# Performance work log

Hardware: AMD Instinct MI355X
Metric: run time of the kernel (lower is better)

The kernel has to match this reference:

```python
import jax, jax.numpy as jnp
import numpy as np

B, T, HOR = 4096, 128, 24
EH, DH, A = 64, 64, 32


def setup_inputs() -> dict:
    key = jax.random.key(0)
    ks = jax.random.split(key, 21)
    g = lambda k, shape, s=0.1: (jax.random.normal(k, shape, jnp.float32) * s)
    return {
        "x": jax.random.normal(ks[0], (B, T, 1), jnp.float32),
        # encoder GRUCell (input_size=1)
        "W_ih_e": g(ks[1], (3 * EH, 1)), "W_hh_e": g(ks[2], (3 * EH, EH)),
        "b_ih_e": g(ks[3], (3 * EH,)), "b_hh_e": g(ks[4], (3 * EH,)),
        # encoder input attention
        "W_e": g(ks[5], (A, EH)), "U_e": g(ks[6], (1, A)),
        "b_e": jnp.zeros((1, A), jnp.float32), "v_e": g(ks[7], (A,)),
        # decoder init
        "W_init": g(ks[8], (DH, EH)), "b_init": g(ks[9], (DH,)),
        # decoder GRUCell (input_size=1)
        "W_ih_d": g(ks[10], (3 * DH, 1)), "W_hh_d": g(ks[11], (3 * DH, DH)),
        "b_ih_d": g(ks[12], (3 * DH,)), "b_hh_d": g(ks[13], (3 * DH,)),
        # temporal attention
        "W_d": g(ks[14], (A, DH)), "U_d": g(ks[15], (A, EH)), "v_d": g(ks[16], (A,)),
        # output head
        "W_out": g(ks[17], (1, DH + EH)), "b_out": g(ks[18], (1,)),
        "y0": jnp.zeros((1,), jnp.float32),
    }


def _gru_cell(x, h, W_ih, W_hh, b_ih, b_hh):
    # PyTorch GRUCell semantics
    gi = x @ W_ih.T + b_ih  # (B, 3H)
    gh = h @ W_hh.T + b_hh
    ir, iz, inn = jnp.split(gi, 3, axis=1)
    hr, hz, hn = jnp.split(gh, 3, axis=1)
    r = jax.nn.sigmoid(ir + hr)
    z = jax.nn.sigmoid(iz + hz)
    n = jnp.tanh(inn + r * hn)
    return (1.0 - z) * n + z * h


def reference(x, W_ih_e, W_hh_e, b_ih_e, b_hh_e, W_e, U_e, b_e, v_e,
              W_init, b_init, W_ih_d, W_hh_d, b_ih_d, b_hh_d,
              W_d, U_d, v_d, W_out, b_out, y0):
    bsz = x.shape[0]

    def enc_step(h, x_t):  # x_t: (B, 1)
        h_proj = h @ W_e.T  # (B, A)
        attn = jnp.tanh(h_proj[:, None, :] + x_t[:, :, None] * U_e[None] + b_e[None])  # (B,1,A)
        scores = jnp.sum(attn * v_e, axis=2)  # (B, 1)
        alpha = jax.nn.softmax(scores, axis=1)
        h_new = _gru_cell(alpha * x_t, h, W_ih_e, W_hh_e, b_ih_e, b_hh_e)
        return h_new, h_new

    h0 = jnp.zeros((bsz, EH), x.dtype)
    h_T, Hs = jax.lax.scan(enc_step, h0, jnp.swapaxes(x, 0, 1))  # Hs: (T,B,EH)
    H = jnp.swapaxes(Hs, 0, 1)  # (B, T, EH)

    d0 = h_T @ W_init.T + b_init  # (B, DH)
    H_proj = jnp.einsum('bte,ae->bta', H, U_d)  # hoisted: constant across decoder steps
    dec_in0 = jnp.broadcast_to(y0[None, :], (bsz, 1))

    def dec_step(carry, _):
        d, dec_in = carry
        d = _gru_cell(dec_in, d, W_ih_d, W_hh_d, b_ih_d, b_hh_d)
        d_proj = d @ W_d.T  # (B, A)
        attn = jnp.tanh(d_proj[:, None, :] + H_proj)  # (B, T, A)
        beta = jax.nn.softmax(jnp.sum(attn * v_d, axis=2), axis=1)  # (B, T)
        ctx = jnp.einsum('bt,bte->be', beta, H)  # (B, EH)
        out = jnp.concatenate([d, ctx], axis=1) @ W_out.T + b_out  # (B, 1)
        return (d, out), out[:, 0]

    (_, _), outs = jax.lax.scan(dec_step, (d0, dec_in0), None, length=HOR)
    return outs.T  # (B, horizon)
```

## Files before the change

kernel.cpp:

```cpp
#include <hip/hip_runtime.h>
#include <math.h>

#define BATCH 4096
#define T 128
#define HOR 24

#define LOG2E 1.44269504088896f
#define C2    2.88539008177793f

typedef _Float16 half2_t __attribute__((ext_vector_type(2)));
typedef _Float16 half8   __attribute__((ext_vector_type(8)));
typedef float f2  __attribute__((ext_vector_type(2)));
typedef float f4v __attribute__((ext_vector_type(4)));

__device__ __forceinline__ float fexp2(float x){ return __builtin_amdgcn_exp2f(x); }
__device__ __forceinline__ float frcp(float x){ return __builtin_amdgcn_rcpf(x); }
__device__ __forceinline__ float fsig(float x){ return frcp(1.0f + fexp2(-LOG2E*x)); }
__device__ __forceinline__ float ftanh(float x){ return fmaf(-2.0f, frcp(1.0f + fexp2(C2*x)), 1.0f); }
__device__ __forceinline__ half2_t bch(unsigned u){ return __builtin_bit_cast(half2_t,u); }
__device__ __forceinline__ unsigned pk2(float a,float b){ return __builtin_bit_cast(unsigned, __builtin_amdgcn_cvt_pkrtz(a,b)); }
__device__ __forceinline__ unsigned pk2rne(float a,float b){
  half2_t h; h.x = (_Float16)a; h.y = (_Float16)b;
  return __builtin_bit_cast(unsigned, h);
}
__device__ __forceinline__ float fdot2f(half2_t a, half2_t b, float c){
#if __has_builtin(__builtin_amdgcn_fdot2)
  return __builtin_amdgcn_fdot2(a,b,c,false);
#else
  return fmaf((float)a.x,(float)b.x, fmaf((float)a.y,(float)b.y,c));
#endif
}
__device__ __forceinline__ f2 pkfma(f2 a, f2 b, f2 c){ return __builtin_elementwise_fma(a,b,c); }

template <int CTRL, int RMASK>
__device__ __forceinline__ float dpp_add(float v) {
  int s = __builtin_amdgcn_update_dpp(0, __builtin_bit_cast(int, v), CTRL, RMASK, 0xf, true);
  return v + __builtin_bit_cast(float, s);
}
__device__ __forceinline__ float wavesum_dpp(float v) {
  v = dpp_add<0x111, 0xf>(v);
  v = dpp_add<0x112, 0xf>(v);
  v = dpp_add<0x114, 0xf>(v);
  v = dpp_add<0x118, 0xf>(v);
  v = dpp_add<0x142, 0xa>(v);
  v = dpp_add<0x143, 0xc>(v);
  return v;
}
__device__ __forceinline__ float rdl63(float v){
  return __builtin_bit_cast(float, __builtin_amdgcn_readlane(__builtin_bit_cast(int, v), 63));
}

#define WG_BARRIER_LDS() do {                                   \
    asm volatile("s_waitcnt lgkmcnt(0)" ::: "memory");          \
    __builtin_amdgcn_s_barrier();                               \
  } while (0)

__device__ __forceinline__ void gru_mv(const _Float16* hrow,
    const unsigned* wr_r, const unsigned* wr_z, const unsigned* wr_n,
    float& ar0, float& ar1, float& az0, float& az1, float& an0, float& an1)
{
  const uint4* hq = (const uint4*)hrow;
  #pragma unroll
  for (int q = 0; q < 8; ++q) {
    uint4 hv = hq[q];
    ar0 = fdot2f(bch(hv.x), bch(wr_r[4*q+0]), ar0);
    az0 = fdot2f(bch(hv.x), bch(wr_z[4*q+0]), az0);
    an0 = fdot2f(bch(hv.x), bch(wr_n[4*q+0]), an0);
    ar1 = fdot2f(bch(hv.y), bch(wr_r[4*q+1]), ar1);
    az1 = fdot2f(bch(hv.y), bch(wr_z[4*q+1]), az1);
    an1 = fdot2f(bch(hv.y), bch(wr_n[4*q+1]), an1);
    ar0 = fdot2f(bch(hv.z), bch(wr_r[4*q+2]), ar0);
    az0 = fdot2f(bch(hv.z), bch(wr_z[4*q+2]), az0);
    an0 = fdot2f(bch(hv.z), bch(wr_n[4*q+2]), an0);
    ar1 = fdot2f(bch(hv.w), bch(wr_r[4*q+3]), ar1);
    az1 = fdot2f(bch(hv.w), bch(wr_z[4*q+3]), az1);
    an1 = fdot2f(bch(hv.w), bch(wr_n[4*q+3]), an1);
  }
}

__device__ __forceinline__ float proj_dot(const _Float16* base, const unsigned* udr)
{
  float acc = 0.f;
  const uint4* hb = (const uint4*)base;
  #pragma unroll
  for (int q = 0; q < 4; ++q) {
    uint4 hv = hb[q];
    acc = fdot2f(bch(hv.x), bch(udr[4*q+0]), acc);
    acc = fdot2f(bch(hv.y), bch(udr[4*q+1]), acc);
    acc = fdot2f(bch(hv.z), bch(udr[4*q+2]), acc);
    acc = fdot2f(bch(hv.w), bch(udr[4*q+3]), acc);
  }
  return acc;
}

__device__ __forceinline__ half8 cvt8(f4v a, f4v b){
  half8 h;
  h[0]=(_Float16)a.x; h[1]=(_Float16)a.y; h[2]=(_Float16)a.z; h[3]=(_Float16)a.w;
  h[4]=(_Float16)b.x; h[5]=(_Float16)b.y; h[6]=(_Float16)b.z; h[7]=(_Float16)b.w;
  return h;
}

__global__ __launch_bounds__(256, 1)
void darnn_enc(const float* __restrict__ x,
               const float* __restrict__ W_ih_e, const float* __restrict__ W_hh_e,
               const float* __restrict__ b_ih_e, const float* __restrict__ b_hh_e,
               const float* __restrict__ U_d, const float* __restrict__ W_out,
               unsigned* __restrict__ hpG, float* __restrict__ hTG)
{
  const int tid = threadIdx.x;
  const int w = tid >> 6;
  const int l = tid & 63;
  const int c = l & 15;
  const int q = l >> 4;
  const int e0 = blockIdx.x * 16;
  const int m0 = 16*w + 4*q;

  __shared__ __align__(16) _Float16 He[2][16*72];
  __shared__ __align__(16) unsigned xw[16*65];
  __shared__ __align__(16) unsigned ehC[2][16*273];

  for (int idx = tid; idx < 16*64; idx += 256) {
    int e = idx >> 6, j = idx & 63;
    f2 g = ((const f2*)(x + (size_t)(e0+e)*T))[j];
    xw[e*65 + j] = pk2(g.x, g.y);
  }
  for (int idx = tid; idx < 576; idx += 256) ((unsigned*)He[0])[idx] = 0;

  half8 Ar[2], Az[2], An[2];
  #pragma unroll
  for (int kap = 0; kap < 2; ++kap) {
    const f4v* pr = (const f4v*)(W_hh_e + (size_t)(16*w + c)*64       + 32*kap + 8*q);
    const f4v* pz = (const f4v*)(W_hh_e + (size_t)(64 + 16*w + c)*64  + 32*kap + 8*q);
    const f4v* pn = (const f4v*)(W_hh_e + (size_t)(128 + 16*w + c)*64 + 32*kap + 8*q);
    Ar[kap] = cvt8(pr[0], pr[1]);
    Az[kap] = cvt8(pz[0], pz[1]);
    An[kap] = cvt8(pn[0], pn[1]);
  }
  half8 AX[2] = {{0,0,0,0,0,0,0,0},{0,0,0,0,0,0,0,0}};
  if (w < 2) {
    #pragma unroll
    for (int kap = 0; kap < 2; ++kap) {
      const f4v* p = (const f4v*)(U_d + (size_t)(16*w + c)*64 + 32*kap + 8*q);
      AX[kap] = cvt8(p[0] * C2, p[1] * C2);
    }
  } else if (w == 2 && c == 0) {
    #pragma unroll
    for (int kap = 0; kap < 2; ++kap) {
      const f4v* p = (const f4v*)(W_out + 64 + 32*kap + 8*q);
      AX[kap] = cvt8(p[0], p[1]);
    }
  }
  f4v wih0 = *(const f4v*)(W_ih_e + m0);
  f4v wih1 = *(const f4v*)(W_ih_e + 64 + m0);
  f4v wih2 = *(const f4v*)(W_ih_e + 128 + m0);
  f4v bb0  = *(const f4v*)(b_ih_e + m0)      + *(const f4v*)(b_hh_e + m0);
  f4v bb1  = *(const f4v*)(b_ih_e + 64 + m0) + *(const f4v*)(b_hh_e + 64 + m0);
  f4v bi2  = *(const f4v*)(b_ih_e + 128 + m0);
  f4v bh2  = *(const f4v*)(b_hh_e + 128 + m0);
  f4v hreg = {0,0,0,0};
  const f4v z4 = {0,0,0,0};

  __syncthreads();

  #pragma unroll 1
  for (int t = 0; t < T; ++t) {
    if ((t & 15) == 1 && t > 16) {
      int cidx = (t - 17) >> 4;
      const unsigned* sbuf = ehC[cidx & 1];
      int t0 = cidx << 4;
      #pragma unroll
      for (int it = 0; it < 17; ++it) {
        int idx = tid + it*256;
        int e = idx / 272;
        int o = idx - e*272;
        hpG[(size_t)(e0+e)*2176 + t0*17 + o] = sbuf[e*273 + o];
      }
    }
    const _Float16* Hc = He[t & 1];
    half8 B0 = __builtin_bit_cast(half8, *(const uint4*)(Hc + c*72 + 8*q));
    half8 B1 = __builtin_bit_cast(half8, *(const uint4*)(Hc + c*72 + 32 + 8*q));
    if (t > 0) {
      unsigned* eb = ehC[((t-1) >> 4) & 1] + c*273 + ((t-1) & 15)*17;
      if (w < 2) {
        f4v cu = __builtin_amdgcn_mfma_f32_16x16x32_f16(AX[0], B0, z4, 0,0,0);
        cu     = __builtin_amdgcn_mfma_f32_16x16x32_f16(AX[1], B1, cu, 0,0,0);
        float x0 = fexp2(fminf(cu[0], 15.5f));
        float x1 = fexp2(fminf(cu[1], 15.5f));
        float x2 = fexp2(fminf(cu[2], 15.5f));
        float x3 = fexp2(fminf(cu[3], 15.5f));
        eb[8*w + 2*q]   = pk2rne(x0, x1);
        eb[8*w + 2*q+1] = pk2rne(x2, x3);
      } else if (w == 2) {
        f4v cw = __builtin_amdgcn_mfma_f32_16x16x32_f16(AX[0], B0, z4, 0,0,0);
        cw     = __builtin_amdgcn_mfma_f32_16x16x32_f16(AX[1], B1, cw, 0,0,0);
        if (q == 0) ((float*)eb)[16] = cw[0];
      }
    }
    f4v gr = __builtin_amdgcn_mfma_f32_16x16x32_f16(Ar[0], B0, z4, 0,0,0);
    gr     = __builtin_amdgcn_mfma_f32_16x16x32_f16(Ar[1], B1, gr, 0,0,0);
    f4v gz = __builtin_amdgcn_mfma_f32_16x16x32_f16(Az[0], B0, z4, 0,0,0);
    gz     = __builtin_amdgcn_mfma_f32_16x16x32_f16(Az[1], B1, gz, 0,0,0);
    f4v gn = __builtin_amdgcn_mfma_f32_16x16x32_f16(An[0], B0, z4, 0,0,0);
    gn     = __builtin_amdgcn_mfma_f32_16x16x32_f16(An[1], B1, gn, 0,0,0);
    float xc = (float)((const _Float16*)xw)[c*130 + t];
    f4v hn;
    #pragma unroll
    for (int i = 0; i < 4; ++i) {
      float r  = fsig(fmaf(xc, wih0[i], bb0[i]) + gr[i]);
      float zf = fsig(fmaf(xc, wih1[i], bb1[i]) + gz[i]);
      float n  = ftanh(fmaf(xc, wih2[i], bi2[i]) + r*(gn[i] + bh2[i]));
      float h  = fmaf(zf, hreg[i] - n, n);
      hreg[i] = h;
      hn[i] = h;
    }
    uint2 wv; wv.x = pk2(hn[0], hn[1]); wv.y = pk2(hn[2], hn[3]);
    *(uint2*)(He[(t+1)&1] + c*72 + m0) = wv;
    WG_BARRIER_LDS();
  }
  {
    const _Float16* Hc = He[0];
    half8 B0 = __builtin_bit_cast(half8, *(const uint4*)(Hc + c*72 + 8*q));
    half8 B1 = __builtin_bit_cast(half8, *(const uint4*)(Hc + c*72 + 32 + 8*q));
    unsigned* eb = ehC[1] + c*273 + 15*17;
    if (w < 2) {
      f4v cu = __builtin_amdgcn_mfma_f32_16x16x32_f16(AX[0], B0, z4, 0,0,0);
      cu     = __builtin_amdgcn_mfma_f32_16x16x32_f16(AX[1], B1, cu, 0,0,0);
      float x0 = fexp2(fminf(cu[0], 15.5f));
      float x1 = fexp2(fminf(cu[1], 15.5f));
      float x2 = fexp2(fminf(cu[2], 15.5f));
      float x3 = fexp2(fminf(cu[3], 15.5f));
      eb[8*w + 2*q]   = pk2rne(x0, x1);
      eb[8*w + 2*q+1] = pk2rne(x2, x3);
    } else if (w == 2) {
      f4v cw = __builtin_amdgcn_mfma_f32_16x16x32_f16(AX[0], B0, z4, 0,0,0);
      cw     = __builtin_amdgcn_mfma_f32_16x16x32_f16(AX[1], B1, cw, 0,0,0);
      if (q == 0) ((float*)eb)[16] = cw[0];
    }
  }
  WG_BARRIER_LDS();
  {
    const unsigned* sbuf = ehC[1];
    #pragma unroll
    for (int it = 0; it < 17; ++it) {
      int idx = tid + it*256;
      int e = idx / 272;
      int o = idx - e*272;
      hpG[(size_t)(e0+e)*2176 + 112*17 + o] = sbuf[e*273 + o];
    }
  }
  #pragma unroll
  for (int i = 0; i < 4; ++i)
    hTG[(size_t)(e0 + c)*64 + m0 + i] = hreg[i];
}

__global__ __launch_bounds__(128, 2)
void darnn_dec(const float* __restrict__ W_init, const float* __restrict__ b_init,
               const float* __restrict__ W_ih_d, const float* __restrict__ W_hh_d,
               const float* __restrict__ b_ih_d, const float* __restrict__ b_hh_d,
               const float* __restrict__ W_d, const float* __restrict__ v_d,
               const float* __restrict__ W_out, const float* __restrict__ b_out,
               const float* __restrict__ y0,
               const unsigned* __restrict__ hpG, const float* __restrict__ hTG,
               float* __restrict__ out)
{
  const int tid = threadIdx.x;
  const int wid = tid >> 6;
  const int l   = tid & 63;
  const int bA  = 4*blockIdx.x + 2*wid;
  const int bB  = bA + 1;
  const int a    = l & 31;
  const int half = l >> 5;

  __shared__ __align__(16) unsigned char smem[36928];
  unsigned char* wbp = smem + wid*18464;
  unsigned* hpA   = (unsigned*)wbp;
  unsigned* hpB   = (unsigned*)(wbp + 8704);
  _Float16* ringA = (_Float16*)(wbp + 17408);
  _Float16* ringB = (_Float16*)(wbp + 17536);
  float*    dpA   = (float*)(wbp + 17664);
  float*    dpB   = (float*)(wbp + 17792);
  float*    hTA   = (float*)(wbp + 17920);
  float*    hTB   = (float*)(wbp + 18176);

  {
    const uint4* sA = (const uint4*)(hpG + (size_t)bA * 2176);
    const uint4* sB = (const uint4*)(hpG + (size_t)bB * 2176);
    #pragma unroll
    for (int it = 0; it < 8; ++it) {
      ((uint4*)hpA)[it*64 + l] = sA[it*64 + l];
      ((uint4*)hpB)[it*64 + l] = sB[it*64 + l];
    }
    const unsigned* rA = hpG + (size_t)bA*2176 + 2048;
    const unsigned* rB = hpG + (size_t)bB*2176 + 2048;
    hpA[2048 + l] = rA[l];      hpA[2112 + l] = rA[64 + l];
    hpB[2048 + l] = rB[l];      hpB[2112 + l] = rB[64 + l];
  }
  hTA[l] = hTG[(size_t)bA*64 + l];
  hTB[l] = hTG[(size_t)bB*64 + l];

  unsigned wr_r[32], wr_z[32], wr_n[32];
  {
    const f4v* wp = (const f4v*)W_hh_d;
    #pragma unroll
    for (int k = 0; k < 16; ++k) {
      f4v vr = wp[l*16 + k];
      f4v vz = wp[(64 + l)*16 + k];
      f4v vn = wp[(128 + l)*16 + k];
      wr_r[2*k] = pk2(vr.x, vr.y); wr_r[2*k+1] = pk2(vr.z, vr.w);
      wr_z[2*k] = pk2(vz.x, vz.y); wr_z[2*k+1] = pk2(vz.z, vz.w);
      wr_n[2*k] = pk2(vn.x, vn.y); wr_n[2*k+1] = pk2(vn.z, vn.w);
    }
  }
  float wih0 = W_ih_d[l], wih1 = W_ih_d[64+l], wih2 = W_ih_d[128+l];
  float bb0  = b_ih_d[l] + b_hh_d[l];
  float bb1  = b_ih_d[64+l] + b_hh_d[64+l];
  float bih2 = b_ih_d[128+l], bhh2 = b_hh_d[128+l];
  unsigned udr[16];
  {
    const f2* up = (const f2*)(W_d + a*64 + half*32);
    #pragma unroll
    for (int k = 0; k < 16; ++k) { f2 f = up[k]; udr[k] = pk2(f.x, f.y); }
  }
  float dprevA, dprevB;
  {
    const f4v* wi = (const f4v*)(W_init + l*64);
    const f4v* ga = (const f4v*)hTA;
    const f4v* gb = (const f4v*)hTB;
    f2 aa0={0,0}, aa1={0,0}, ba0={0,0}, ba1={0,0};
    #pragma unroll
    for (int k = 0; k < 16; ++k) {
      f4v wv = wi[k];
      f4v va = ga[k], vb = gb[k];
      aa0 = pkfma(wv.xy, va.xy, aa0);
      aa1 = pkfma(wv.zw, va.zw, aa1);
      ba0 = pkfma(wv.xy, vb.xy, ba0);
      ba1 = pkfma(wv.zw, vb.zw, ba1);
    }
    float bi = b_init[l];
    dprevA = bi + (aa0.x + aa0.y) + (aa1.x + aa1.y);
    dprevB = bi + (ba0.x + ba0.y) + (ba1.x + ba1.y);
  }
  float wout1 = W_out[l];
  float hw0A = __builtin_bit_cast(float, hpA[l*17 + 16]);
  float hw1A = __builtin_bit_cast(float, hpA[(64 + l)*17 + 16]);
  float hw0B = __builtin_bit_cast(float, hpB[l*17 + 16]);
  float hw1B = __builtin_bit_cast(float, hpB[(64 + l)*17 + 16]);
  float oprevA = y0[0], oprevB = y0[0];
  float bo = b_out[0];
  float c1;
  {
    float sv = v_d[a];
    sv += __shfl_xor(sv, 16); sv += __shfl_xor(sv, 8);
    sv += __shfl_xor(sv, 4);  sv += __shfl_xor(sv, 2); sv += __shfl_xor(sv, 1);
    c1 = LOG2E * sv;
  }
  ringA[l] = (_Float16)dprevA;
  ringB[l] = (_Float16)dprevB;

  const unsigned* hprA0 = hpA + l*17;
  const unsigned* hprA1 = hpA + (64 + l)*17;
  const unsigned* hprB0 = hpB + l*17;
  const unsigned* hprB1 = hpB + (64 + l)*17;

  #pragma unroll 1
  for (int s = 0; s < HOR; ++s) {
    float ar0A=0,ar1A=0,az0A=0,az1A=0,an0A=0,an1A=0;
    float ar0B=0,ar1B=0,az0B=0,az1B=0,an0B=0,an1B=0;
    gru_mv(ringA, wr_r, wr_z, wr_n, ar0A,ar1A,az0A,az1A,an0A,an1A);
    gru_mv(ringB, wr_r, wr_z, wr_n, ar0B,ar1B,az0B,az1B,an0B,an1B);
    float rA = fsig(fmaf(oprevA, wih0, bb0) + ar0A + ar1A);
    float zA = fsig(fmaf(oprevA, wih1, bb1) + az0A + az1A);
    float nA = ftanh(fmaf(oprevA, wih2, bih2) + rA * (an0A + an1A + bhh2));
    float dnewA = fmaf(zA, dprevA - nA, nA);
    float rB = fsig(fmaf(oprevB, wih0, bb0) + ar0B + ar1B);
    float zB = fsig(fmaf(oprevB, wih1, bb1) + az0B + az1B);
    float nB = ftanh(fmaf(oprevB, wih2, bih2) + rB * (an0B + an1B + bhh2));
    float dnewB = fmaf(zB, dprevB - nB, nB);
    dprevA = dnewA; dprevB = dnewB;
    ringA[l] = (_Float16)dnewA;
    ringB[l] = (_Float16)dnewB;
    {
      float accA = proj_dot(ringA + half*32, udr);
      float accB = proj_dot(ringB + half*32, udr);
      accA += __shfl_xor(accA, 32);
      accB += __shfl_xor(accB, 32);
      if (l < 32) {
        dpA[l] = fexp2(C2 * accA);
        dpB[l] = fexp2(C2 * accB);
      }
    }
    float rs0A = 0.f, rs1A = 0.f, rs0B = 0.f, rs1B = 0.f;
    #pragma unroll
    for (int j2 = 0; j2 < 8; ++j2) {
      f4v edA = *(const f4v*)&dpA[4*j2];
      f4v edB = *(const f4v*)&dpB[4*j2];
      half2_t haA0 = bch(hprA0[2*j2]), hbA0 = bch(hprA0[2*j2+1]);
      half2_t haA1 = bch(hprA1[2*j2]), hbA1 = bch(hprA1[2*j2+1]);
      half2_t haB0 = bch(hprB0[2*j2]), hbB0 = bch(hprB0[2*j2+1]);
      half2_t haB1 = bch(hprB1[2*j2]), hbB1 = bch(hprB1[2*j2+1]);
      float v0 = v_d[4*j2], v1 = v_d[4*j2+1], v2 = v_d[4*j2+2], v3 = v_d[4*j2+3];
      rs0A = fmaf(v0, frcp(fmaf(edA.x, (float)haA0.x, 1.0f)), rs0A);
      rs0B = fmaf(v0, frcp(fmaf(edB.x, (float)haB0.x, 1.0f)), rs0B);
      rs0A = fmaf(v1, frcp(fmaf(edA.y, (float)haA0.y, 1.0f)), rs0A);
      rs0B = fmaf(v1, frcp(fmaf(edB.y, (float)haB0.y, 1.0f)), rs0B);
      rs0A = fmaf(v2, frcp(fmaf(edA.z, (float)hbA0.x, 1.0f)), rs0A);
      rs0B = fmaf(v2, frcp(fmaf(edB.z, (float)hbB0.x, 1.0f)), rs0B);
      rs0A = fmaf(v3, frcp(fmaf(edA.w, (float)hbA0.y, 1.0f)), rs0A);
      rs0B = fmaf(v3, frcp(fmaf(edB.w, (float)hbB0.y, 1.0f)), rs0B);
      rs1A = fmaf(v0, frcp(fmaf(edA.x, (float)haA1.x, 1.0f)), rs1A);
      rs1B = fmaf(v0, frcp(fmaf(edB.x, (float)haB1.x, 1.0f)), rs1B);
      rs1A = fmaf(v1, frcp(fmaf(edA.y, (float)haA1.y, 1.0f)), rs1A);
      rs1B = fmaf(v1, frcp(fmaf(edB.y, (float)haB1.y, 1.0f)), rs1B);
      rs1A = fmaf(v2, frcp(fmaf(edA.z, (float)hbA1.x, 1.0f)), rs1A);
      rs1B = fmaf(v2, frcp(fmaf(edB.z, (float)hbB1.x, 1.0f)), rs1B);
      rs1A = fmaf(v3, frcp(fmaf(edA.w, (float)hbA1.y, 1.0f)), rs1A);
      rs1B = fmaf(v3, frcp(fmaf(edB.w, (float)hbB1.y, 1.0f)), rs1B);
    }
    float e0A = fexp2(fmaf(-C2, rs0A, c1));
    float e1A = fexp2(fmaf(-C2, rs1A, c1));
    float e0B = fexp2(fmaf(-C2, rs0B, c1));
    float e1B = fexp2(fmaf(-C2, rs1B, c1));
    float P0A = rdl63(wavesum_dpp(e0A + e1A));
    float P1A = rdl63(wavesum_dpp(fmaf(e0A, hw0A, e1A * hw1A)));
    float P2A = rdl63(wavesum_dpp(wout1 * dnewA));
    float P0B = rdl63(wavesum_dpp(e0B + e1B));
    float P1B = rdl63(wavesum_dpp(fmaf(e0B, hw0B, e1B * hw1B)));
    float P2B = rdl63(wavesum_dpp(wout1 * dnewB));
    float oA = fmaf(P1A, frcp(P0A), P2A + bo);
    float oB = fmaf(P1B, frcp(P0B), P2B + bo);
    if (l == 0) {
      out[(size_t)bA * HOR + s] = oA;
      out[(size_t)bB * HOR + s] = oB;
    }
    oprevA = oA; oprevB = oB;
  }
}

extern "C" void kernel_launch(void* const* d_in, const int* in_sizes, int n_in,
                              void* d_out, int out_size, void* d_ws, size_t ws_size,
                              hipStream_t stream) {
  const float* x      = (const float*)d_in[0];
  const float* W_ih_e = (const float*)d_in[1];
  const float* W_hh_e = (const float*)d_in[2];
  const float* b_ih_e = (const float*)d_in[3];
  const float* b_hh_e = (const float*)d_in[4];
  const float* W_init = (const float*)d_in[9];
  const float* b_init = (const float*)d_in[10];
  const float* W_ih_d = (const float*)d_in[11];
  const float* W_hh_d = (const float*)d_in[12];
  const float* b_ih_d = (const float*)d_in[13];
  const float* b_hh_d = (const float*)d_in[14];
  const float* W_d    = (const float*)d_in[15];
  const float* U_d    = (const float*)d_in[16];
  const float* v_d    = (const float*)d_in[17];
  const float* W_out  = (const float*)d_in[18];
  const float* b_out  = (const float*)d_in[19];
  const float* y0     = (const float*)d_in[20];
  float* outp = (float*)d_out;

  unsigned* hpG = (unsigned*)d_ws;
  float*    hTG = (float*)((char*)d_ws + (size_t)BATCH * 2176 * 4);

  darnn_enc<<<BATCH/16, 256, 0, stream>>>(x, W_ih_e, W_hh_e, b_ih_e, b_hh_e,
      U_d, W_out, hpG, hTG);
  darnn_dec<<<BATCH/4, 128, 0, stream>>>(W_init, b_init, W_ih_d, W_hh_d,
      b_ih_d, b_hh_d, W_d, v_d, W_out, b_out, y0, hpG, hTG, outp);
}
```

Baseline: 272.1 us.

## Collapse encoder workgroup to one wave computing all hidden tiles without barriers

The encoder now runs one 64-lane wave per 16-sequence block instead of four waves. That single wave does all four gate row tiles plus the attention-projection MFMAs, so the per-step workgroup barrier and the double-buffered hidden state disappear. The projected keys are written straight to global memory each step instead of being staged in LDS and flushed in 16-step chunks. In exchange, each wave's serial dependency chain per step grows about fourfold, CU occupancy drops to one wave, and the global stores become small and strided rather than coalesced.

```diff
diff --git a/kernel.cpp b/kernel.cpp
--- a/kernel.cpp
+++ b/kernel.cpp
@@ -23,6 +23,7 @@
   half2_t h; h.x = (_Float16)a; h.y = (_Float16)b;
   return __builtin_bit_cast(unsigned, h);
 }
+__device__ __forceinline__ float e2c(float v){ return fexp2(fminf(v, 15.5f)); }
 __device__ __forceinline__ float fdot2f(half2_t a, half2_t b, float c){
 #if __has_builtin(__builtin_amdgcn_fdot2)
   return __builtin_amdgcn_fdot2(a,b,c,false);
@@ -49,11 +50,6 @@
 __device__ __forceinline__ float rdl63(float v){
   return __builtin_bit_cast(float, __builtin_amdgcn_readlane(__builtin_bit_cast(int, v), 63));
 }
-
-#define WG_BARRIER_LDS() do {                                   \
-    asm volatile("s_waitcnt lgkmcnt(0)" ::: "memory");          \
-    __builtin_amdgcn_s_barrier();                               \
-  } while (0)
 
 __device__ __forceinline__ void gru_mv(const _Float16* hrow,
     const unsigned* wr_r, const unsigned* wr_z, const unsigned* wr_n,
@@ -100,157 +96,139 @@
   return h;
 }
 
-__global__ __launch_bounds__(256, 1)
+__global__ __launch_bounds__(64, 1)
 void darnn_enc(const float* __restrict__ x,
                const float* __restrict__ W_ih_e, const float* __restrict__ W_hh_e,
                const float* __restrict__ b_ih_e, const float* __restrict__ b_hh_e,
                const float* __restrict__ U_d, const float* __restrict__ W_out,
                unsigned* __restrict__ hpG, float* __restrict__ hTG)
 {
-  const int tid = threadIdx.x;
-  const int w = tid >> 6;
-  const int l = tid & 63;
+  const int l = threadIdx.x;
   const int c = l & 15;
   const int q = l >> 4;
   const int e0 = blockIdx.x * 16;
-  const int m0 = 16*w + 4*q;
-
-  __shared__ __align__(16) _Float16 He[2][16*72];
+
+  __shared__ __align__(16) unsigned He[16*68];
   __shared__ __align__(16) unsigned xw[16*65];
-  __shared__ __align__(16) unsigned ehC[2][16*273];
-
-  for (int idx = tid; idx < 16*64; idx += 256) {
+
+  for (int idx = l; idx < 16*64; idx += 64) {
     int e = idx >> 6, j = idx & 63;
     f2 g = ((const f2*)(x + (size_t)(e0+e)*T))[j];
     xw[e*65 + j] = pk2(g.x, g.y);
   }
-  for (int idx = tid; idx < 576; idx += 256) ((unsigned*)He[0])[idx] = 0;
-
-  half8 Ar[2], Az[2], An[2];
-  #pragma unroll
-  for (int kap = 0; kap < 2; ++kap) {
-    const f4v* pr = (const f4v*)(W_hh_e + (size_t)(16*w + c)*64       + 32*kap + 8*q);
-    const f4v* pz = (const f4v*)(W_hh_e + (size_t)(64 + 16*w + c)*64  + 32*kap + 8*q);
-    const f4v* pn = (const f4v*)(W_hh_e + (size_t)(128 + 16*w + c)*64 + 32*kap + 8*q);
-    Ar[kap] = cvt8(pr[0], pr[1]);
-    Az[kap] = cvt8(pz[0], pz[1]);
-    An[kap] = cvt8(pn[0], pn[1]);
-  }
-  half8 AX[2] = {{0,0,0,0,0,0,0,0},{0,0,0,0,0,0,0,0}};
-  if (w < 2) {
+  #pragma unroll
+  for (int it = 0; it < 17; ++it) He[l + it*64] = 0;
+
+  half8 Ar[4][2], Az[4][2], An[4][2];
+  #pragma unroll
+  for (int M = 0; M < 4; ++M) {
     #pragma unroll
     for (int kap = 0; kap < 2; ++kap) {
-      const f4v* p = (const f4v*)(U_d + (size_t)(16*w + c)*64 + 32*kap + 8*q);
-      AX[kap] = cvt8(p[0] * C2, p[1] * C2);
-    }
-  } else if (w == 2 && c == 0) {
+      const f4v* pr = (const f4v*)(W_hh_e + (size_t)(16*M + c)*64       + 32*kap + 8*q);
+      const f4v* pz = (const f4v*)(W_hh_e + (size_t)(64 + 16*M + c)*64  + 32*kap + 8*q);
+      const f4v* pn = (const f4v*)(W_hh_e + (size_t)(128 + 16*M + c)*64 + 32*kap + 8*q);
+      Ar[M][kap] = cvt8(pr[0], pr[1]);
+      Az[M][kap] = cvt8(pz[0], pz[1]);
+      An[M][kap] = cvt8(pn[0], pn[1]);
+    }
+  }
+  half8 AX[2][2], AW[2];
+  #pragma unroll
+  for (int M = 0; M < 2; ++M) {
+    #pragma unroll
+    for (int kap = 0; kap < 2; ++kap) {
+      const f4v* p = (const f4v*)(U_d + (size_t)(16*M + c)*64 + 32*kap + 8*q);
+      AX[M][kap] = cvt8(p[0] * C2, p[1] * C2);
+    }
+  }
+  AW[0] = (half8){0,0,0,0,0,0,0,0};
+  AW[1] = (half8){0,0,0,0,0,0,0,0};
+  if (c == 0) {
     #pragma unroll
     for (int kap = 0; kap < 2; ++kap) {
       const f4v* p = (const f4v*)(W_out + 64 + 32*kap + 8*q);
-      AX[kap] = cvt8(p[0], p[1]);
-    }
-  }
-  f4v wih0 = *(const f4v*)(W_ih_e + m0);
-  f4v wih1 = *(const f4v*)(W_ih_e + 64 + m0);
-  f4v wih2 = *(const f4v*)(W_ih_e + 128 + m0);
-  f4v bb0  = *(const f4v*)(b_ih_e + m0)      + *(const f4v*)(b_hh_e + m0);
-  f4v bb1  = *(const f4v*)(b_ih_e + 64 + m0) + *(const f4v*)(b_hh_e + 64 + m0);
-  f4v bi2  = *(const f4v*)(b_ih_e + 128 + m0);
-  f4v bh2  = *(const f4v*)(b_hh_e + 128 + m0);
-  f4v hreg = {0,0,0,0};
+      AW[kap] = cvt8(p[0], p[1]);
+    }
+  }
+  f4v wih0[4], wih1[4], wih2[4], bb0[4], bb1[4], bi2[4], bh2[4];
+  #pragma unroll
+  for (int M = 0; M < 4; ++M) {
+    int m0 = 16*M + 4*q;
+    wih0[M] = *(const f4v*)(W_ih_e + m0);
+    wih1[M] = *(const f4v*)(W_ih_e + 64 + m0);
+    wih2[M] = *(const f4v*)(W_ih_e + 128 + m0);
+    bb0[M]  = *(const f4v*)(b_ih_e + m0)      + *(const f4v*)(b_hh_e + m0);
+    bb1[M]  = *(const f4v*)(b_ih_e + 64 + m0) + *(const f4v*)(b_hh_e + 64 + m0);
+    bi2[M]  = *(const f4v*)(b_ih_e + 128 + m0);
+    bh2[M]  = *(const f4v*)(b_hh_e + 128 + m0);
+  }
+  f4v hreg[4] = {{0,0,0,0},{0,0,0,0},{0,0,0,0},{0,0,0,0}};
   const f4v z4 = {0,0,0,0};
-
-  __syncthreads();
+  unsigned* hpB = hpG + (size_t)(e0 + c) * 2176;
 
   #pragma unroll 1
   for (int t = 0; t < T; ++t) {
-    if ((t & 15) == 1 && t > 16) {
-      int cidx = (t - 17) >> 4;
-      const unsigned* sbuf = ehC[cidx & 1];
-      int t0 = cidx << 4;
+    half8 B0 = __builtin_bit_cast(half8, *(const uint4*)&He[c*68 + 4*q]);
+    half8 B1 = __builtin_bit_cast(half8, *(const uint4*)&He[c*68 + 16 + 4*q]);
+    if (t > 0) {
+      f4v cu0 = __builtin_amdgcn_mfma_f32_16x16x32_f16(AX[0][0], B0, z4, 0,0,0);
+      cu0     = __builtin_amdgcn_mfma_f32_16x16x32_f16(AX[0][1], B1, cu0, 0,0,0);
+      f4v cu1 = __builtin_amdgcn_mfma_f32_16x16x32_f16(AX[1][0], B0, z4, 0,0,0);
+      cu1     = __builtin_amdgcn_mfma_f32_16x16x32_f16(AX[1][1], B1, cu1, 0,0,0);
+      f4v cw  = __builtin_amdgcn_mfma_f32_16x16x32_f16(AW[0],    B0, z4, 0,0,0);
+      cw      = __builtin_amdgcn_mfma_f32_16x16x32_f16(AW[1],    B1, cw, 0,0,0);
+      unsigned* hpE = hpB + (t-1)*17;
+      hpE[2*q]     = pk2rne(e2c(cu0[0]), e2c(cu0[1]));
+      hpE[2*q+1]   = pk2rne(e2c(cu0[2]), e2c(cu0[3]));
+      hpE[8+2*q]   = pk2rne(e2c(cu1[0]), e2c(cu1[1]));
+      hpE[8+2*q+1] = pk2rne(e2c(cu1[2]), e2c(cu1[3]));
+      if (q == 0) ((float*)hpE)[16] = cw[0];
+    }
+    float xc = (float)((const _Float16*)xw)[c*130 + t];
+    #pragma unroll
+    for (int M = 0; M < 4; ++M) {
+      f4v gr = __builtin_amdgcn_mfma_f32_16x16x32_f16(Ar[M][0], B0, z4, 0,0,0);
+      gr     = __builtin_amdgcn_mfma_f32_16x16x32_f16(Ar[M][1], B1, gr, 0,0,0);
+      f4v gz = __builtin_amdgcn_mfma_f32_16x16x32_f16(Az[M][0], B0, z4, 0,0,0);
+      gz     = __builtin_amdgcn_mfma_f32_16x16x32_f16(Az[M][1], B1, gz, 0,0,0);
+      f4v gn = __builtin_amdgcn_mfma_f32_16x16x32_f16(An[M][0], B0, z4, 0,0,0);
+      gn     = __builtin_amdgcn_mfma_f32_16x16x32_f16(An[M][1], B1, gn, 0,0,0);
+      f4v hn;
       #pragma unroll
-      for (int it = 0; it < 17; ++it) {
-        int idx = tid + it*256;
-        int e = idx / 272;
-        int o = idx - e*272;
-        hpG[(size_t)(e0+e)*2176 + t0*17 + o] = sbuf[e*273 + o];
+      for (int i = 0; i < 4; ++i) {
+        float r  = fsig(fmaf(xc, wih0[M][i], bb0[M][i]) + gr[i]);
+        float zf = fsig(fmaf(xc, wih1[M][i], bb1[M][i]) + gz[i]);
+        float n  = ftanh(fmaf(xc, wih2[M][i], bi2[M][i]) + r*(gn[i] + bh2[M][i]));
+        float h  = fmaf(zf, hreg[M][i] - n, n);
+        hreg[M][i] = h;
+        hn[i] = h;
       }
-    }
-    const _Float16* Hc = He[t & 1];
-    half8 B0 = __builtin_bit_cast(half8, *(const uint4*)(Hc + c*72 + 8*q));
-    half8 B1 = __builtin_bit_cast(half8, *(const uint4*)(Hc + c*72 + 32 + 8*q));
-    if (t > 0) {
-      unsigned* eb = ehC[((t-1) >> 4) & 1] + c*273 + ((t-1) & 15)*17;
-      if (w < 2) {
-        f4v cu = __builtin_amdgcn_mfma_f32_16x16x32_f16(AX[0], B0, z4, 0,0,0);
-        cu     = __builtin_amdgcn_mfma_f32_16x16x32_f16(AX[1], B1, cu, 0,0,0);
-        float x0 = fexp2(fminf(cu[0], 15.5f));
-        float x1 = fexp2(fminf(cu[1], 15.5f));
-        float x2 = fexp2(fminf(cu[2], 15.5f));
-        float x3 = fexp2(fminf(cu[3], 15.5f));
-        eb[8*w + 2*q]   = pk2rne(x0, x1);
-        eb[8*w + 2*q+1] = pk2rne(x2, x3);
-      } else if (w == 2) {
-        f4v cw = __builtin_amdgcn_mfma_f32_16x16x32_f16(AX[0], B0, z4, 0,0,0);
-        cw     = __builtin_amdgcn_mfma_f32_16x16x32_f16(AX[1], B1, cw, 0,0,0);
-        if (q == 0) ((float*)eb)[16] = cw[0];
-      }
-    }
-    f4v gr = __builtin_amdgcn_mfma_f32_16x16x32_f16(Ar[0], B0, z4, 0,0,0);
-    gr     = __builtin_amdgcn_mfma_f32_16x16x32_f16(Ar[1], B1, gr, 0,0,0);
-    f4v gz = __builtin_amdgcn_mfma_f32_16x16x32_f16(Az[0], B0, z4, 0,0,0);
-    gz     = __builtin_amdgcn_mfma_f32_16x16x32_f16(Az[1], B1, gz, 0,0,0);
-    f4v gn = __builtin_amdgcn_mfma_f32_16x16x32_f16(An[0], B0, z4, 0,0,0);
-    gn     = __builtin_amdgcn_mfma_f32_16x16x32_f16(An[1], B1, gn, 0,0,0);
-    float xc = (float)((const _Float16*)xw)[c*130 + t];
-    f4v hn;
-    #pragma unroll
-    for (int i = 0; i < 4; ++i) {
-      float r  = fsig(fmaf(xc, wih0[i], bb0[i]) + gr[i]);
-      float zf = fsig(fmaf(xc, wih1[i], bb1[i]) + gz[i]);
-      float n  = ftanh(fmaf(xc, wih2[i], bi2[i]) + r*(gn[i] + bh2[i]));
-      float h  = fmaf(zf, hreg[i] - n, n);
-      hreg[i] = h;
-      hn[i] = h;
-    }
-    uint2 wv; wv.x = pk2(hn[0], hn[1]); wv.y = pk2(hn[2], hn[3]);
-    *(uint2*)(He[(t+1)&1] + c*72 + m0) = wv;
-    WG_BARRIER_LDS();
-  }
-  {
-    const _Float16* Hc = He[0];
-    half8 B0 = __builtin_bit_cast(half8, *(const uint4*)(Hc + c*72 + 8*q));
-    half8 B1 = __builtin_bit_cast(half8, *(const uint4*)(Hc + c*72 + 32 + 8*q));
-    unsigned* eb = ehC[1] + c*273 + 15*17;
-    if (w < 2) {
-      f4v cu = __builtin_amdgcn_mfma_f32_16x16x32_f16(AX[0], B0, z4, 0,0,0);
-      cu     = __builtin_amdgcn_mfma_f32_16x16x32_f16(AX[1], B1, cu, 0,0,0);
-      float x0 = fexp2(fminf(cu[0], 15.5f));
-      float x1 = fexp2(fminf(cu[1], 15.5f));
-      float x2 = fexp2(fminf(cu[2], 15.5f));
-      float x3 = fexp2(fminf(cu[3], 15.5f));
-      eb[8*w + 2*q]   = pk2rne(x0, x1);
-      eb[8*w + 2*q+1] = pk2rne(x2, x3);
-    } else if (w == 2) {
-      f4v cw = __builtin_amdgcn_mfma_f32_16x16x32_f16(AX[0], B0, z4, 0,0,0);
-      cw     = __builtin_amdgcn_mfma_f32_16x16x32_f16(AX[1], B1, cw, 0,0,0);
-      if (q == 0) ((float*)eb)[16] = cw[0];
-    }
-  }
-  WG_BARRIER_LDS();
-  {
-    const unsigned* sbuf = ehC[1];
-    #pragma unroll
-    for (int it = 0; it < 17; ++it) {
-      int idx = tid + it*256;
-      int e = idx / 272;
-      int o = idx - e*272;
-      hpG[(size_t)(e0+e)*2176 + 112*17 + o] = sbuf[e*273 + o];
-    }
-  }
-  #pragma unroll
-  for (int i = 0; i < 4; ++i)
-    hTG[(size_t)(e0 + c)*64 + m0 + i] = hreg[i];
+      uint2 wv; wv.x = pk2(hn[0], hn[1]); wv.y = pk2(hn[2], hn[3]);
+      *(uint2*)&He[c*68 + 8*M + 2*q] = wv;
+    }
+  }
+  {
+    half8 B0 = __builtin_bit_cast(half8, *(const uint4*)&He[c*68 + 4*q]);
+    half8 B1 = __builtin_bit_cast(half8, *(const uint4*)&He[c*68 + 16 + 4*q]);
+    f4v cu0 = __builtin_amdgcn_mfma_f32_16x16x32_f16(AX[0][0], B0, z4, 0,0,0);
+    cu0     = __builtin_amdgcn_mfma_f32_16x16x32_f16(AX[0][1], B1, cu0, 0,0,0);
+    f4v cu1 = __builtin_amdgcn_mfma_f32_16x16x32_f16(AX[1][0], B0, z4, 0,0,0);
+    cu1     = __builtin_amdgcn_mfma_f32_16x16x32_f16(AX[1][1], B1, cu1, 0,0,0);
+    f4v cw  = __builtin_amdgcn_mfma_f32_16x16x32_f16(AW[0],    B0, z4, 0,0,0);
+    cw      = __builtin_amdgcn_mfma_f32_16x16x32_f16(AW[1],    B1, cw, 0,0,0);
+    unsigned* hpE = hpB + 127*17;
+    hpE[2*q]     = pk2rne(e2c(cu0[0]), e2c(cu0[1]));
+    hpE[2*q+1]   = pk2rne(e2c(cu0[2]), e2c(cu0[3]));
+    hpE[8+2*q]   = pk2rne(e2c(cu1[0]), e2c(cu1[1]));
+    hpE[8+2*q+1] = pk2rne(e2c(cu1[2]), e2c(cu1[3]));
+    if (q == 0) ((float*)hpE)[16] = cw[0];
+  }
+  #pragma unroll
+  for (int M = 0; M < 4; ++M) {
+    #pragma unroll
+    for (int i = 0; i < 4; ++i)
+      hTG[(size_t)(e0 + c)*64 + 16*M + 4*q + i] = hreg[M][i];
+  }
 }
 
 __global__ __launch_bounds__(128, 2)
@@ -461,7 +439,7 @@
   unsigned* hpG = (unsigned*)d_ws;
   float*    hTG = (float*)((char*)d_ws + (size_t)BATCH * 2176 * 4);
 
-  darnn_enc<<<BATCH/16, 256, 0, stream>>>(x, W_ih_e, W_hh_e, b_ih_e, b_hh_e,
+  darnn_enc<<<BATCH/16, 64, 0, stream>>>(x, W_ih_e, W_hh_e, b_ih_e, b_hh_e,
       U_d, W_out, hpG, hTG);
   darnn_dec<<<BATCH/4, 128, 0, stream>>>(W_init, b_init, W_ih_d, W_hh_d,
       b_ih_d, b_hh_d, W_d, v_d, W_out, b_out, y0, hpG, hTG, outp);
```

Result: slower. 369.5 us (+35.8%).

## Write encoder projections straight to global and hold decoder H-proj in registers

Applied to the files above, without the earlier changes.

The encoder no longer stages its per-step exp(U_d·h) and W_out·h values in a shared-memory ring that is flushed to global every 16 steps. Each lane now writes its values directly to global memory, which drops the staging buffer, the periodic copy loops and the final barrier. The decoder no longer copies each row's projected-H block into shared memory. Each lane loads its 4×17 words into registers, and the decoder's shared memory shrinks from about 36 KB to about 2 KB. The cost is scattered small global stores inside the encoder's serial loop and higher register pressure in the decoder, which could cause spills or lower occupancy.

```diff
diff --git a/kernel.cpp b/kernel.cpp
--- a/kernel.cpp
+++ b/kernel.cpp
@@ -117,7 +117,6 @@
 
   __shared__ __align__(16) _Float16 He[2][16*72];
   __shared__ __align__(16) unsigned xw[16*65];
-  __shared__ __align__(16) unsigned ehC[2][16*273];
 
   for (int idx = tid; idx < 16*64; idx += 256) {
     int e = idx >> 6, j = idx & 63;
@@ -159,41 +158,30 @@
   f4v bh2  = *(const f4v*)(b_hh_e + 128 + m0);
   f4v hreg = {0,0,0,0};
   const f4v z4 = {0,0,0,0};
+  unsigned* hpB = hpG + (size_t)(e0 + c) * 2176;
 
   __syncthreads();
 
   #pragma unroll 1
   for (int t = 0; t < T; ++t) {
-    if ((t & 15) == 1 && t > 16) {
-      int cidx = (t - 17) >> 4;
-      const unsigned* sbuf = ehC[cidx & 1];
-      int t0 = cidx << 4;
-      #pragma unroll
-      for (int it = 0; it < 17; ++it) {
-        int idx = tid + it*256;
-        int e = idx / 272;
-        int o = idx - e*272;
-        hpG[(size_t)(e0+e)*2176 + t0*17 + o] = sbuf[e*273 + o];
-      }
-    }
     const _Float16* Hc = He[t & 1];
     half8 B0 = __builtin_bit_cast(half8, *(const uint4*)(Hc + c*72 + 8*q));
     half8 B1 = __builtin_bit_cast(half8, *(const uint4*)(Hc + c*72 + 32 + 8*q));
     if (t > 0) {
-      unsigned* eb = ehC[((t-1) >> 4) & 1] + c*273 + ((t-1) & 15)*17;
       if (w < 2) {
         f4v cu = __builtin_amdgcn_mfma_f32_16x16x32_f16(AX[0], B0, z4, 0,0,0);
         cu     = __builtin_amdgcn_mfma_f32_16x16x32_f16(AX[1], B1, cu, 0,0,0);
+        unsigned* hpE = hpB + (t-1)*17 + 8*w;
         float x0 = fexp2(fminf(cu[0], 15.5f));
         float x1 = fexp2(fminf(cu[1], 15.5f));
         float x2 = fexp2(fminf(cu[2], 15.5f));
         float x3 = fexp2(fminf(cu[3], 15.5f));
-        eb[8*w + 2*q]   = pk2rne(x0, x1);
-        eb[8*w + 2*q+1] = pk2rne(x2, x3);
+        hpE[2*q]   = pk2rne(x0, x1);
+        hpE[2*q+1] = pk2rne(x2, x3);
       } else if (w == 2) {
         f4v cw = __builtin_amdgcn_mfma_f32_16x16x32_f16(AX[0], B0, z4, 0,0,0);
         cw     = __builtin_amdgcn_mfma_f32_16x16x32_f16(AX[1], B1, cw, 0,0,0);
-        if (q == 0) ((float*)eb)[16] = cw[0];
+        if (q == 0) ((float*)(hpB + (t-1)*17))[16] = cw[0];
       }
     }
     f4v gr = __builtin_amdgcn_mfma_f32_16x16x32_f16(Ar[0], B0, z4, 0,0,0);
@@ -221,31 +209,20 @@
     const _Float16* Hc = He[0];
     half8 B0 = __builtin_bit_cast(half8, *(const uint4*)(Hc + c*72 + 8*q));
     half8 B1 = __builtin_bit_cast(half8, *(const uint4*)(Hc + c*72 + 32 + 8*q));
-    unsigned* eb = ehC[1] + c*273 + 15*17;
     if (w < 2) {
       f4v cu = __builtin_amdgcn_mfma_f32_16x16x32_f16(AX[0], B0, z4, 0,0,0);
       cu     = __builtin_amdgcn_mfma_f32_16x16x32_f16(AX[1], B1, cu, 0,0,0);
+      unsigned* hpE = hpB + 127*17 + 8*w;
       float x0 = fexp2(fminf(cu[0], 15.5f));
       float x1 = fexp2(fminf(cu[1], 15.5f));
       float x2 = fexp2(fminf(cu[2], 15.5f));
       float x3 = fexp2(fminf(cu[3], 15.5f));
-      eb[8*w + 2*q]   = pk2rne(x0, x1);
-      eb[8*w + 2*q+1] = pk2rne(x2, x3);
+      hpE[2*q]   = pk2rne(x0, x1);
+      hpE[2*q+1] = pk2rne(x2, x3);
     } else if (w == 2) {
       f4v cw = __builtin_amdgcn_mfma_f32_16x16x32_f16(AX[0], B0, z4, 0,0,0);
       cw     = __builtin_amdgcn_mfma_f32_16x16x32_f16(AX[1], B1, cw, 0,0,0);
-      if (q == 0) ((float*)eb)[16] = cw[0];
-    }
-  }
-  WG_BARRIER_LDS();
-  {
-    const unsigned* sbuf = ehC[1];
-    #pragma unroll
-    for (int it = 0; it < 17; ++it) {
-      int idx = tid + it*256;
-      int e = idx / 272;
-      int o = idx - e*272;
-      hpG[(size_t)(e0+e)*2176 + 112*17 + o] = sbuf[e*273 + o];
+      if (q == 0) ((float*)(hpB + 127*17))[16] = cw[0];
     }
   }
   #pragma unroll
@@ -271,29 +248,26 @@
   const int a    = l & 31;
   const int half = l >> 5;
 
-  __shared__ __align__(16) unsigned char smem[36928];
-  unsigned char* wbp = smem + wid*18464;
-  unsigned* hpA   = (unsigned*)wbp;
-  unsigned* hpB   = (unsigned*)(wbp + 8704);
-  _Float16* ringA = (_Float16*)(wbp + 17408);
-  _Float16* ringB = (_Float16*)(wbp + 17536);
-  float*    dpA   = (float*)(wbp + 17664);
-  float*    dpB   = (float*)(wbp + 17792);
-  float*    hTA   = (float*)(wbp + 17920);
-  float*    hTB   = (float*)(wbp + 18176);
-
-  {
-    const uint4* sA = (const uint4*)(hpG + (size_t)bA * 2176);
-    const uint4* sB = (const uint4*)(hpG + (size_t)bB * 2176);
-    #pragma unroll
-    for (int it = 0; it < 8; ++it) {
-      ((uint4*)hpA)[it*64 + l] = sA[it*64 + l];
-      ((uint4*)hpB)[it*64 + l] = sB[it*64 + l];
-    }
-    const unsigned* rA = hpG + (size_t)bA*2176 + 2048;
-    const unsigned* rB = hpG + (size_t)bB*2176 + 2048;
-    hpA[2048 + l] = rA[l];      hpA[2112 + l] = rA[64 + l];
-    hpB[2048 + l] = rB[l];      hpB[2112 + l] = rB[64 + l];
+  __shared__ __align__(16) unsigned char smem[2304];
+  unsigned char* wbp = smem + wid*1152;
+  _Float16* ringA = (_Float16*)wbp;
+  _Float16* ringB = (_Float16*)(wbp + 128);
+  float*    dpA   = (float*)(wbp + 256);
+  float*    dpB   = (float*)(wbp + 384);
+  float*    hTA   = (float*)(wbp + 512);
+  float*    hTB   = (float*)(wbp + 768);
+
+  unsigned hrA0[17], hrA1[17], hrB0[17], hrB1[17];
+  {
+    const unsigned* pA0 = hpG + (size_t)bA*2176 + l*17;
+    const unsigned* pA1 = hpG + (size_t)bA*2176 + (64+l)*17;
+    const unsigned* pB0 = hpG + (size_t)bB*2176 + l*17;
+    const unsigned* pB1 = hpG + (size_t)bB*2176 + (64+l)*17;
+    #pragma unroll
+    for (int k = 0; k < 17; ++k) {
+      hrA0[k] = pA0[k]; hrA1[k] = pA1[k];
+      hrB0[k] = pB0[k]; hrB1[k] = pB1[k];
+    }
   }
   hTA[l] = hTG[(size_t)bA*64 + l];
   hTB[l] = hTG[(size_t)bB*64 + l];
@@ -341,10 +315,10 @@
     dprevB = bi + (ba0.x + ba0.y) + (ba1.x + ba1.y);
   }
   float wout1 = W_out[l];
-  float hw0A = __builtin_bit_cast(float, hpA[l*17 + 16]);
-  float hw1A = __builtin_bit_cast(float, hpA[(64 + l)*17 + 16]);
-  float hw0B = __builtin_bit_cast(float, hpB[l*17 + 16]);
-  float hw1B = __builtin_bit_cast(float, hpB[(64 + l)*17 + 16]);
+  float hw0A = __builtin_bit_cast(float, hrA0[16]);
+  float hw1A = __builtin_bit_cast(float, hrA1[16]);
+  float hw0B = __builtin_bit_cast(float, hrB0[16]);
+  float hw1B = __builtin_bit_cast(float, hrB1[16]);
   float oprevA = y0[0], oprevB = y0[0];
   float bo = b_out[0];
   float c1;
@@ -356,11 +330,6 @@
   }
   ringA[l] = (_Float16)dprevA;
   ringB[l] = (_Float16)dprevB;
-
-  const unsigned* hprA0 = hpA + l*17;
-  const unsigned* hprA1 = hpA + (64 + l)*17;
-  const unsigned* hprB0 = hpB + l*17;
-  const unsigned* hprB1 = hpB + (64 + l)*17;
 
   #pragma unroll 1
   for (int s = 0; s < HOR; ++s) {
@@ -394,10 +363,10 @@
     for (int j2 = 0; j2 < 8; ++j2) {
       f4v edA = *(const f4v*)&dpA[4*j2];
       f4v edB = *(const f4v*)&dpB[4*j2];
-      half2_t haA0 = bch(hprA0[2*j2]), hbA0 = bch(hprA0[2*j2+1]);
-      half2_t haA1 = bch(hprA1[2*j2]), hbA1 = bch(hprA1[2*j2+1]);
-      half2_t haB0 = bch(hprB0[2*j2]), hbB0 = bch(hprB0[2*j2+1]);
-      half2_t haB1 = bch(hprB1[2*j2]), hbB1 = bch(hprB1[2*j2+1]);
+      half2_t haA0 = bch(hrA0[2*j2]), hbA0 = bch(hrA0[2*j2+1]);
+      half2_t haA1 = bch(hrA1[2*j2]), hbA1 = bch(hrA1[2*j2+1]);
+      half2_t haB0 = bch(hrB0[2*j2]), hbB0 = bch(hrB0[2*j2+1]);
+      half2_t haB1 = bch(hrB1[2*j2]), hbB1 = bch(hrB1[2*j2+1]);
       float v0 = v_d[4*j2], v1 = v_d[4*j2+1], v2 = v_d[4*j2+2], v3 = v_d[4*j2+3];
       rs0A = fmaf(v0, frcp(fmaf(edA.x, (float)haA0.x, 1.0f)), rs0A);
       rs0B = fmaf(v0, frcp(fmaf(edB.x, (float)haB0.x, 1.0f)), rs0B);
```

Result: slower. 312.4 us (+14.8%).
